# Optimization experiments

Hardware: AMD Instinct MI355X
Metric: run time of the kernel (lower is better)

## Reference

```python
import jax, jax.numpy as jnp
import numpy as np

NF = 2560          # number of pyramid filters
TW = 16            # filter_temporal_width
H = W = 96
B, T = 8, 240
# center_idx = ceil(TW/2)-1 = 7 -> pad_left = TW-1-7 = 8, pad_right = 7
PAD_L, PAD_R = 8, 7
EPS = 1e-5
MASK_KEEP = 0.35   # approximate Gabor support fraction


def setup_inputs() -> dict:
    key = jax.random.key(0)
    ks = jax.random.split(key, 6)
    x = jax.random.normal(ks[0], (B, T, H, W), dtype=jnp.float32)
    w_s_sin = jax.random.normal(ks[1], (NF, H, W), dtype=jnp.float32)
    w_s_cos = jax.random.normal(ks[2], (NF, H, W), dtype=jnp.float32)
    # emulate the Gabor support mask (weights zeroed outside support)
    mask = (jax.random.uniform(ks[3], (NF, H, W)) < MASK_KEEP).astype(jnp.float32)
    w_s_sin = w_s_sin * mask
    w_s_cos = w_s_cos * mask
    w_t_sin = jax.random.normal(ks[4], (NF, TW), dtype=jnp.float32)
    w_t_cos = jax.random.normal(ks[5], (NF, TW), dtype=jnp.float32)
    return {"x": x, "w_s_sin": w_s_sin, "w_s_cos": w_s_cos,
            "w_t_sin": w_t_sin, "w_t_cos": w_t_cos}


def _dwconv1d(g, w):
    # g: (B, NF, T); w: (NF, TW) already time-flipped (cross-correlation),
    # depthwise conv with groups = NF, 'same'-style asymmetric padding.
    return jax.lax.conv_general_dilated(
        g, w[:, None, :], window_strides=(1,), padding=[(PAD_L, PAD_R)],
        dimension_numbers=("NCH", "OIH", "NCH"), feature_group_count=NF)


def reference(x, w_s_sin, w_s_cos, w_t_sin, w_t_cos):
    # full-frame spatial conv2d == contraction over (H, W): (B,T,NF)
    g_sin = jnp.einsum("bthw,fhw->bft", x, w_s_sin)  # (B, NF, T)
    g_cos = jnp.einsum("bthw,fhw->bft", x, w_s_cos)
    term1 = _dwconv1d(g_sin, w_t_cos)
    term2 = _dwconv1d(g_cos, w_t_sin)
    term3 = _dwconv1d(g_cos, w_t_cos)
    term4 = _dwconv1d(g_sin, w_t_sin)
    resp_sin = term1 + term2
    resp_cos = term3 - term4
    energy = jnp.log(jnp.sqrt(resp_sin * resp_sin + resp_cos * resp_cos) + EPS)
    return jnp.transpose(energy, (0, 2, 1))  # (B, T, NF)
```

## Files before the change

kernel.cpp:

```cpp
#include <hip/hip_runtime.h>

#define T_LEN   240
#define B_SZ    8
#define NFILT   2560
#define KD      9216
#define M_DIM   1920
#define N_DIM   5120
#define PAD_L   8
#define KSPLIT  3
#define KSLICE  3072
#define NT      96
#define GEMM_LDS 131072

typedef unsigned short u16;
typedef __attribute__((ext_vector_type(8)))  __bf16 bf16x8;
typedef __attribute__((ext_vector_type(16))) float  f32x16;

__device__ __forceinline__ u16 f2bf_rne(float f) {
    unsigned u = __float_as_uint(f);
    u += 0x7FFFu + ((u >> 16) & 1u);
    return (u16)(u >> 16);
}

__device__ __forceinline__ void split4(const float* __restrict__ src,
                                       u16* __restrict__ hi, u16* __restrict__ lo, int i) {
    const float4 v = ((const float4*)src)[i];
    float vv[4] = {v.x, v.y, v.z, v.w};
    u16 hh[4], ll[4];
#pragma unroll
    for (int j = 0; j < 4; ++j) {
        unsigned u = __float_as_uint(vv[j]);
        unsigned r = u + 0x7FFFu + ((u >> 16) & 1u);
        u16 hb = (u16)(r >> 16);
        float hf = __uint_as_float((unsigned)hb << 16);
        hh[j] = hb;
        ll[j] = f2bf_rne(vv[j] - hf);
    }
    ushort4 h, l;
    h.x = hh[0]; h.y = hh[1]; h.z = hh[2]; h.w = hh[3];
    l.x = ll[0]; l.y = ll[1]; l.z = ll[2]; l.w = ll[3];
    ((ushort4*)hi)[i] = h;
    ((ushort4*)lo)[i] = l;
}

#define NX4  (17694720 / 4)
#define NW4  (23592960 / 4)
#define NG4  (9830400 / 4)
__global__ void split_all_kernel(const float* __restrict__ x,
                                 const float* __restrict__ wss,
                                 const float* __restrict__ wsc,
                                 u16* __restrict__ xh, u16* __restrict__ xl,
                                 u16* __restrict__ wh, u16* __restrict__ wl,
                                 float* __restrict__ g) {
    int i = blockIdx.x * 256 + threadIdx.x;
    if (i < NX4) {
        split4(x, xh, xl, i);
    } else if (i < NX4 + NW4) {
        split4(wss, wh, wl, i - NX4);
    } else if (i < NX4 + 2 * NW4) {
        int j = i - NX4 - NW4;
        split4(wsc, wh + (size_t)NFILT * KD, wl + (size_t)NFILT * KD, j);
    }
    if (i < NG4) {
        float4 z; z.x = 0.f; z.y = 0.f; z.z = 0.f; z.w = 0.f;
        ((float4*)g)[i] = z;
    }
}

__device__ __forceinline__ void glds16(const u16* gp, __bf16* lp) {
    __builtin_amdgcn_global_load_lds(
        (const __attribute__((address_space(1))) void*)gp,
        (__attribute__((address_space(3))) void*)lp, 16, 0, 0);
}

__device__ __forceinline__ int frag_off(int r, int fo) {
    return r * 32 + (((fo >> 3) ^ ((r >> 1) & 3)) << 3);
}

__global__ __launch_bounds__(512, 2) void gemm_split_kernel(
    const u16* __restrict__ xh, const u16* __restrict__ xl,
    const u16* __restrict__ wh, const u16* __restrict__ wl,
    float* __restrict__ g) {

    extern __shared__ char smem_c[];
    __bf16* const smem = (__bf16*)smem_c;

    const int tid = threadIdx.x;
    const int l   = tid & 63;
    const int w   = tid >> 6;

    int bid = (int)blockIdx.x;
    bid = (bid & 7) * (160 * KSPLIT / 8) + (bid >> 3);
    const int ks = bid / 160;
    const int t  = bid % 160;
    const int m0 = (t / 20) * 256;
    const int n0 = (t % 20) * 256;
    const unsigned kb = (unsigned)ks * KSLICE;

    const int rl  = w * 16 + (l >> 2);
    const int gsw = ((l & 3) ^ ((rl >> 1) & 3)) * 8;
    const int sd  = w * 512 + l * 8;

    int ar0 = m0 + rl;        if (ar0 > M_DIM - 1) ar0 = M_DIM - 1;
    int ar1 = m0 + rl + 128;  if (ar1 > M_DIM - 1) ar1 = M_DIM - 1;
    const unsigned offA0 = (unsigned)ar0 * KD + kb + gsw;
    const unsigned offA1 = (unsigned)ar1 * KD + kb + gsw;
    const unsigned offB0 = (unsigned)(n0 + rl) * KD + kb + gsw;
    const unsigned offB1 = (unsigned)(n0 + rl + 128) * KD + kb + gsw;

#define ST_BH(D,KO) do { __bf16* s_ = smem + (D)*32768;                 \
        glds16(wh + (offB0 + (KO)), s_ + 16384 + sd);                   \
        glds16(wh + (offB1 + (KO)), s_ + 20480 + sd); } while (0)
#define ST_BL(D,KO) do { __bf16* s_ = smem + (D)*32768;                 \
        glds16(wl + (offB0 + (KO)), s_ + 24576 + sd);                   \
        glds16(wl + (offB1 + (KO)), s_ + 28672 + sd); } while (0)
#define ST_A0(D,KO) do { __bf16* s_ = smem + (D)*32768;                 \
        glds16(xh + (offA0 + (KO)), s_ + 0     + sd);                   \
        glds16(xl + (offA0 + (KO)), s_ + 8192  + sd); } while (0)
#define ST_A1(D,KO) do { __bf16* s_ = smem + (D)*32768;                 \
        glds16(xh + (offA1 + (KO)), s_ + 4096  + sd);                   \
        glds16(xl + (offA1 + (KO)), s_ + 12288 + sd); } while (0)

    const int rA = l & 31;
    const int kq = (l >> 5) * 8;
    const int wr = w >> 2;
    const int wc = w & 3;

    int aoff[2][2][2], boff[2][2];
#pragma unroll
    for (int h = 0; h < 2; ++h)
#pragma unroll
        for (int mf = 0; mf < 2; ++mf)
#pragma unroll
            for (int s = 0; s < 2; ++s)
                aoff[h][mf][s] = frag_off(h * 128 + wr * 64 + mf * 32 + rA, s * 16 + kq);
#pragma unroll
    for (int nf = 0; nf < 2; ++nf)
#pragma unroll
        for (int s = 0; s < 2; ++s)
            boff[nf][s] = frag_off(wc * 64 + nf * 32 + rA, s * 16 + kq);

    f32x16 acc[4][2];
#pragma unroll
    for (int i = 0; i < 4; ++i)
#pragma unroll
        for (int j = 0; j < 2; ++j)
#pragma unroll
            for (int r = 0; r < 16; ++r)
                acc[i][j][r] = 0.f;

#define MFMA3(ACC, AH, AL, BH, BL)                                              \
    ACC = __builtin_amdgcn_mfma_f32_32x32x16_bf16(AH, BH, ACC, 0, 0, 0);        \
    ACC = __builtin_amdgcn_mfma_f32_32x32x16_bf16(AH, BL, ACC, 0, 0, 0);        \
    ACC = __builtin_amdgcn_mfma_f32_32x32x16_bf16(AL, BH, ACC, 0, 0, 0);

#define MFMA_CLUSTER(H, S) do {                                                 \
        __builtin_amdgcn_s_setprio(1);                                          \
        MFMA3(acc[(H)*2 + 0][0], ah_[0], al_[0], bh_[0][S], bl_[0][S]);         \
        MFMA3(acc[(H)*2 + 0][1], ah_[0], al_[0], bh_[1][S], bl_[1][S]);         \
        MFMA3(acc[(H)*2 + 1][0], ah_[1], al_[1], bh_[0][S], bl_[0][S]);         \
        MFMA3(acc[(H)*2 + 1][1], ah_[1], al_[1], bh_[1][S], bl_[1][S]);         \
        __builtin_amdgcn_s_setprio(0);                                          \
    } while (0)

#define LOAD_A(H, S) do {                                                       \
        ah_[0] = *(const bf16x8*)(sb + aoff[H][0][S]);                          \
        ah_[1] = *(const bf16x8*)(sb + aoff[H][1][S]);                          \
        al_[0] = *(const bf16x8*)(sb + 8192 + aoff[H][0][S]);                   \
        al_[1] = *(const bf16x8*)(sb + 8192 + aoff[H][1][S]);                   \
    } while (0)

#define SYNC_IN() do {                                                          \
        __builtin_amdgcn_s_barrier();                                           \
        asm volatile("s_waitcnt lgkmcnt(0)" ::: "memory");                      \
        __builtin_amdgcn_sched_barrier(0);                                      \
    } while (0)

    ST_BH(0, 0); ST_BL(0, 0); ST_A0(0, 0); ST_A1(0, 0);
    asm volatile("s_waitcnt vmcnt(2)" ::: "memory");
    __builtin_amdgcn_s_barrier();

    for (int kt = 0; kt < NT; ++kt) {
        const int cur = kt & 1;
        const int nxt = cur ^ 1;
        const __bf16* sb = smem + cur * 32768;
        const int ko = (kt + 1) * 32;
        const bool pf = (kt < NT - 1);

        bf16x8 bh_[2][2], bl_[2][2], ah_[2], al_[2];

#pragma unroll
        for (int nf = 0; nf < 2; ++nf)
#pragma unroll
            for (int s = 0; s < 2; ++s) {
                bh_[nf][s] = *(const bf16x8*)(sb + 16384 + boff[nf][s]);
                bl_[nf][s] = *(const bf16x8*)(sb + 24576 + boff[nf][s]);
            }
        LOAD_A(0, 0);
        if (pf) ST_BH(nxt, ko);
        SYNC_IN();
        MFMA_CLUSTER(0, 0);
        __builtin_amdgcn_s_barrier();

        LOAD_A(0, 1);
        if (pf) ST_BL(nxt, ko);
        SYNC_IN();
        MFMA_CLUSTER(0, 1);
        if (pf) { asm volatile("s_waitcnt vmcnt(4)" ::: "memory"); }
        else    { asm volatile("s_waitcnt vmcnt(0)" ::: "memory"); }
        __builtin_amdgcn_s_barrier();

        LOAD_A(1, 0);
        if (pf) ST_A0(nxt, ko);
        SYNC_IN();
        MFMA_CLUSTER(1, 0);
        __builtin_amdgcn_s_barrier();

        LOAD_A(1, 1);
        if (pf) ST_A1(nxt, ko);
        SYNC_IN();
        MFMA_CLUSTER(1, 1);
        if (pf) { asm volatile("s_waitcnt vmcnt(2)" ::: "memory"); }
        __builtin_amdgcn_s_barrier();
    }

    const int cb = (l >> 5) * 4;
    const int cc = l & 31;
#pragma unroll
    for (int am = 0; am < 4; ++am) {
        const int rowb = m0 + (am >> 1) * 128 + wr * 64 + (am & 1) * 32;
        if (rowb < M_DIM) {
#pragma unroll
            for (int nf = 0; nf < 2; ++nf) {
                const int col = n0 + wc * 64 + nf * 32 + cc;
                float* gp = g + (size_t)rowb * N_DIM + col;
#pragma unroll
                for (int r = 0; r < 16; ++r) {
                    const int ro = (r & 3) + 8 * (r >> 2) + cb;
                    atomicAdd(gp + (size_t)ro * N_DIM, acc[am][nf][r]);
                }
            }
        }
    }
#undef ST_BH
#undef ST_BL
#undef ST_A0
#undef ST_A1
#undef MFMA3
#undef MFMA_CLUSTER
#undef LOAD_A
#undef SYNC_IN
}

__global__ __launch_bounds__(256) void conv_energy_kernel(
    const float* __restrict__ g,
    const float* __restrict__ wts,
    const float* __restrict__ wtc,
    float* __restrict__ out) {

    __shared__ float wl_c[16][256];
    __shared__ float wl_s[16][256];

    const int tid = threadIdx.x;
    const int bid = blockIdx.x;
    const int fc  = bid % 10;
    const int t   = (bid / 10) % T_LEN;
    const int b   = bid / (10 * T_LEN);
    const int f0  = fc * 256;

    {
        const float4* wrc = (const float4*)(wtc + (size_t)(f0 + tid) * 16);
        const float4* wrs = (const float4*)(wts + (size_t)(f0 + tid) * 16);
#pragma unroll
        for (int k4 = 0; k4 < 4; ++k4) {
            const float4 vc = wrc[k4];
            const float4 vs = wrs[k4];
            wl_c[k4 * 4 + 0][tid] = vc.x; wl_c[k4 * 4 + 1][tid] = vc.y;
            wl_c[k4 * 4 + 2][tid] = vc.z; wl_c[k4 * 4 + 3][tid] = vc.w;
            wl_s[k4 * 4 + 0][tid] = vs.x; wl_s[k4 * 4 + 1][tid] = vs.y;
            wl_s[k4 * 4 + 2][tid] = vs.z; wl_s[k4 * 4 + 3][tid] = vs.w;
        }
    }
    __syncthreads();

    const float* grow = g + (size_t)b * T_LEN * N_DIM + f0 + tid;
    float s = 0.f, c = 0.f;
#pragma unroll
    for (int j = 0; j < 16; ++j) {
        const int tt = t + j - PAD_L;
        if (tt >= 0 && tt < T_LEN) {
            const float gs = grow[(size_t)tt * N_DIM];
            const float gc = grow[(size_t)tt * N_DIM + NFILT];
            const float a  = wl_c[j][tid];
            const float bb = wl_s[j][tid];
            s += gs * a + gc * bb;
            c += gc * a - gs * bb;
        }
    }
    const float r = sqrtf(s * s + c * c);
    out[(size_t)((b * T_LEN + t) * NFILT) + f0 + tid] = logf(r + 1e-5f);
}

extern "C" void kernel_launch(void* const* d_in, const int* in_sizes, int n_in,
                              void* d_out, int out_size, void* d_ws, size_t ws_size,
                              hipStream_t stream) {
    const float* x   = (const float*)d_in[0];
    const float* wss = (const float*)d_in[1];
    const float* wsc = (const float*)d_in[2];
    const float* wts = (const float*)d_in[3];
    const float* wtc = (const float*)d_in[4];
    float* out = (float*)d_out;

    char* ws = (char*)d_ws;
    u16*   xh  = (u16*)(ws);
    u16*   xl  = (u16*)(ws + 35389440);
    u16*   whi = (u16*)(ws + 70778880);
    u16*   wlo = (u16*)(ws + 165150720);
    float* g   = (float*)(ws + 259522560);

    static bool gemm_attr_set = false;
    if (!gemm_attr_set) {
        hipFuncSetAttribute(reinterpret_cast<const void*>(gemm_split_kernel),
                            hipFuncAttributeMaxDynamicSharedMemorySize, GEMM_LDS);
        gemm_attr_set = true;
    }

    const int ntot4 = NX4 + 2 * NW4;
    split_all_kernel<<<(ntot4 + 255) / 256, 256, 0, stream>>>(x, wss, wsc, xh, xl, whi, wlo, g);

    gemm_split_kernel<<<160 * KSPLIT, 512, GEMM_LDS, stream>>>(xh, xl, whi, wlo, g);

    conv_energy_kernel<<<B_SZ * T_LEN * 10, 256, 0, stream>>>(g, wts, wtc, out);
}
```

Baseline: 889.9 us.

## Merge GEMM k-step into two phases and skip MFMAs for empty M half

Restructures the GEMM main loop from four barrier-separated phases into two. Each phase issues its global-to-LDS prefetches up front, loads the A and B fragments for both k sub-steps, then runs one long MFMA burst at raised priority. This removes the inner SYNC_IN barriers and lgkmcnt waits. It also adds a per-block flag that skips the second 128-row half of MFMAs and LDS reads when that half lies beyond M=1920 (the last M tile row). In exchange it holds more fragment registers live and leaves less interleaving of LDS reads with MFMA issue.

```diff
diff --git a/kernel.cpp b/kernel.cpp
--- a/kernel.cpp
+++ b/kernel.cpp
@@ -96,6 +96,7 @@
     const int m0 = (t / 20) * 256;
     const int n0 = (t % 20) * 256;
     const unsigned kb = (unsigned)ks * KSLICE;
+    const bool mhalf = (m0 + 128 >= M_DIM);
 
     const int rl  = w * 16 + (l >> 2);
     const int gsw = ((l & 3) ^ ((rl >> 1) & 3)) * 8;
@@ -154,28 +155,6 @@
     ACC = __builtin_amdgcn_mfma_f32_32x32x16_bf16(AH, BL, ACC, 0, 0, 0);        \
     ACC = __builtin_amdgcn_mfma_f32_32x32x16_bf16(AL, BH, ACC, 0, 0, 0);
 
-#define MFMA_CLUSTER(H, S) do {                                                 \
-        __builtin_amdgcn_s_setprio(1);                                          \
-        MFMA3(acc[(H)*2 + 0][0], ah_[0], al_[0], bh_[0][S], bl_[0][S]);         \
-        MFMA3(acc[(H)*2 + 0][1], ah_[0], al_[0], bh_[1][S], bl_[1][S]);         \
-        MFMA3(acc[(H)*2 + 1][0], ah_[1], al_[1], bh_[0][S], bl_[0][S]);         \
-        MFMA3(acc[(H)*2 + 1][1], ah_[1], al_[1], bh_[1][S], bl_[1][S]);         \
-        __builtin_amdgcn_s_setprio(0);                                          \
-    } while (0)
-
-#define LOAD_A(H, S) do {                                                       \
-        ah_[0] = *(const bf16x8*)(sb + aoff[H][0][S]);                          \
-        ah_[1] = *(const bf16x8*)(sb + aoff[H][1][S]);                          \
-        al_[0] = *(const bf16x8*)(sb + 8192 + aoff[H][0][S]);                   \
-        al_[1] = *(const bf16x8*)(sb + 8192 + aoff[H][1][S]);                   \
-    } while (0)
-
-#define SYNC_IN() do {                                                          \
-        __builtin_amdgcn_s_barrier();                                           \
-        asm volatile("s_waitcnt lgkmcnt(0)" ::: "memory");                      \
-        __builtin_amdgcn_sched_barrier(0);                                      \
-    } while (0)
-
     ST_BH(0, 0); ST_BL(0, 0); ST_A0(0, 0); ST_A1(0, 0);
     asm volatile("s_waitcnt vmcnt(2)" ::: "memory");
     __builtin_amdgcn_s_barrier();
@@ -187,39 +166,56 @@
         const int ko = (kt + 1) * 32;
         const bool pf = (kt < NT - 1);
 
-        bf16x8 bh_[2][2], bl_[2][2], ah_[2], al_[2];
-
-#pragma unroll
-        for (int nf = 0; nf < 2; ++nf)
-#pragma unroll
-            for (int s = 0; s < 2; ++s) {
+        bf16x8 bh_[2][2], bl_[2][2], ah_[2][2], al_[2][2];
+
+        if (pf) { ST_BH(nxt, ko); ST_BL(nxt, ko); }
+#pragma unroll
+        for (int s = 0; s < 2; ++s) {
+#pragma unroll
+            for (int nf = 0; nf < 2; ++nf) {
                 bh_[nf][s] = *(const bf16x8*)(sb + 16384 + boff[nf][s]);
                 bl_[nf][s] = *(const bf16x8*)(sb + 24576 + boff[nf][s]);
             }
-        LOAD_A(0, 0);
-        if (pf) ST_BH(nxt, ko);
-        SYNC_IN();
-        MFMA_CLUSTER(0, 0);
-        __builtin_amdgcn_s_barrier();
-
-        LOAD_A(0, 1);
-        if (pf) ST_BL(nxt, ko);
-        SYNC_IN();
-        MFMA_CLUSTER(0, 1);
+#pragma unroll
+            for (int mf = 0; mf < 2; ++mf) {
+                ah_[mf][s] = *(const bf16x8*)(sb + aoff[0][mf][s]);
+                al_[mf][s] = *(const bf16x8*)(sb + 8192 + aoff[0][mf][s]);
+            }
+        }
+        __builtin_amdgcn_s_setprio(1);
+#pragma unroll
+        for (int s = 0; s < 2; ++s)
+#pragma unroll
+            for (int mf = 0; mf < 2; ++mf)
+#pragma unroll
+                for (int nf = 0; nf < 2; ++nf) {
+                    MFMA3(acc[mf][nf], ah_[mf][s], al_[mf][s], bh_[nf][s], bl_[nf][s]);
+                }
+        __builtin_amdgcn_s_setprio(0);
         if (pf) { asm volatile("s_waitcnt vmcnt(4)" ::: "memory"); }
         else    { asm volatile("s_waitcnt vmcnt(0)" ::: "memory"); }
         __builtin_amdgcn_s_barrier();
 
-        LOAD_A(1, 0);
-        if (pf) ST_A0(nxt, ko);
-        SYNC_IN();
-        MFMA_CLUSTER(1, 0);
-        __builtin_amdgcn_s_barrier();
-
-        LOAD_A(1, 1);
-        if (pf) ST_A1(nxt, ko);
-        SYNC_IN();
-        MFMA_CLUSTER(1, 1);
+        if (pf) { ST_A0(nxt, ko); ST_A1(nxt, ko); }
+        if (!mhalf) {
+#pragma unroll
+            for (int s = 0; s < 2; ++s)
+#pragma unroll
+                for (int mf = 0; mf < 2; ++mf) {
+                    ah_[mf][s] = *(const bf16x8*)(sb + aoff[1][mf][s]);
+                    al_[mf][s] = *(const bf16x8*)(sb + 8192 + aoff[1][mf][s]);
+                }
+            __builtin_amdgcn_s_setprio(1);
+#pragma unroll
+            for (int s = 0; s < 2; ++s)
+#pragma unroll
+                for (int mf = 0; mf < 2; ++mf)
+#pragma unroll
+                    for (int nf = 0; nf < 2; ++nf) {
+                        MFMA3(acc[2 + mf][nf], ah_[mf][s], al_[mf][s], bh_[nf][s], bl_[nf][s]);
+                    }
+            __builtin_amdgcn_s_setprio(0);
+        }
         if (pf) { asm volatile("s_waitcnt vmcnt(2)" ::: "memory"); }
         __builtin_amdgcn_s_barrier();
     }
@@ -247,9 +243,6 @@
 #undef ST_A0
 #undef ST_A1
 #undef MFMA3
-#undef MFMA_CLUSTER
-#undef LOAD_A
-#undef SYNC_IN
 }
 
 __global__ __launch_bounds__(256) void conv_energy_kernel(
```

After: 879.8 us. Within noise of the previous version (-1.1%).
